# Performance work log

Hardware: AMD Instinct MI355X
Metric: run time of the kernel (lower is better)

Reference implementation:

```python
import jax, jax.numpy as jnp
import numpy as np

B, S, D = 2, 2048, 1024
H, DH = 16, 64          # n_heads, d_head = d_model // n_heads
WINDOW = 128            # sliding-window size (causal, includes self)


def setup_inputs() -> dict:
    key = jax.random.key(0)
    k1, k2, k3 = jax.random.split(key, 3)
    x = jax.random.normal(k1, (B, S, D), dtype=jnp.float32)
    w_qkv = jax.random.normal(k2, (D, 3 * D), dtype=jnp.float32) * (1.0 / np.sqrt(D))
    w_out = jax.random.normal(k3, (D, D), dtype=jnp.float32) * (1.0 / np.sqrt(D))
    return {"x": x, "w_qkv": w_qkv, "w_out": w_out}


def reference(x, w_qkv, w_out):
    b, s, d = x.shape
    # QKV projection (no bias): [B,S,3D] -> [B,S,3,H,DH]
    qkv = (x @ w_qkv).reshape(b, s, 3, H, DH)
    q, k, v = qkv[:, :, 0], qkv[:, :, 1], qkv[:, :, 2]  # each [B,S,H,DH]
    scale = 1.0 / np.sqrt(DH)
    # Dense scores [B,H,S,S], as the explicit-mask SDPA path computes
    scores = jnp.einsum("bihd,bjhd->bhij", q, k) * scale
    i = jnp.arange(s)[:, None]
    j = jnp.arange(s)[None, :]
    # allowed: causal AND within sliding window of WINDOW positions (incl. self)
    allowed = (j <= i) & (j > i - WINDOW)
    scores = jnp.where(allowed, scores, -jnp.inf)
    attn = jax.nn.softmax(scores, axis=-1)
    out = jnp.einsum("bhij,bjhd->bihd", attn, v).reshape(b, s, d)
    return out @ w_out
```

## Files before the change

kernel.cpp:

```cpp
#include <hip/hip_runtime.h>

#define SQ      2048
#define NB      2
#define NH      16
#define DHD     64
#define WIN     128
#define DMODEL  1024
#define TRIPLE  3072

typedef __attribute__((ext_vector_type(8))) short  short8;
typedef __attribute__((ext_vector_type(4))) float  f32x4;

__device__ __forceinline__ unsigned short f2bf(float f) {
  unsigned u = __float_as_uint(f);
  u += 0x7fff + ((u >> 16) & 1);
  return (unsigned short)(u >> 16);
}

__device__ __forceinline__ void load_lds16(const void* g, void* l) {
  __builtin_amdgcn_global_load_lds(
      (const __attribute__((address_space(1))) unsigned int*)g,
      (__attribute__((address_space(3))) unsigned int*)l, 16, 0, 0);
}

__global__ __launch_bounds__(256) void prep_kernel(
    const float* __restrict__ x, const float* __restrict__ w_qkv,
    const float* __restrict__ w_out,
    unsigned short* __restrict__ xb, unsigned short* __restrict__ wqkvT,
    unsigned short* __restrict__ woutT) {
  __shared__ float tile[32][33];
  int blk = blockIdx.x, tid = threadIdx.x;
  if (blk < 4096) {
    int idx = blk * 256 + tid;
    f32x4 v = ((const f32x4*)x)[idx];
    ushort4 o;
    o.x = f2bf(v[0]); o.y = f2bf(v[1]); o.z = f2bf(v[2]); o.w = f2bf(v[3]);
    ((ushort4*)xb)[idx] = o;
    return;
  }
  const float* in;
  unsigned short* out;
  int K = DMODEL, N, t;
  if (blk < 7168) { in = w_qkv; out = wqkvT; N = TRIPLE;  t = blk - 4096; }
  else            { in = w_out; out = woutT; N = DMODEL;  t = blk - 7168; }
  int ntiles = N / 32;
  int n0 = (t % ntiles) * 32, k0 = (t / ntiles) * 32;
  int tx = tid & 31, ty = tid >> 5;
#pragma unroll
  for (int r = 0; r < 4; ++r)
    tile[ty + 8 * r][tx] = in[(size_t)(k0 + ty + 8 * r) * N + (n0 + tx)];
  __syncthreads();
#pragma unroll
  for (int r = 0; r < 4; ++r)
    out[(size_t)(n0 + ty + 8 * r) * K + (k0 + tx)] = f2bf(tile[tx][ty + 8 * r]);
}

template <bool BF16OUT>
__global__ __launch_bounds__(512) void gemm_bt_kernel(
    const unsigned short* __restrict__ A,
    const unsigned short* __restrict__ Bt,
    void* __restrict__ Cv,
    int M, int N, int K) {
  __shared__ short lsA[128 * 64];
  __shared__ short lsB[128 * 64];
  int tid  = threadIdx.x;
  int wave = tid >> 6, lane = tid & 63;
  int quad = lane >> 4, l16 = lane & 15;
  int wm = (wave & 3) * 32;
  int wn = (wave >> 2) * 64;
  int m0 = blockIdx.x * 128, n0 = blockIdx.y * 128;

  f32x4 acc[2][4] = {};

  const short* Ag = (const short*)A;
  const short* Bg = (const short*)Bt;

  int row8 = lane >> 3;
  int gcol = ((lane & 7) ^ row8) * 8;
  int sw = (l16 & 7) * 8;

  for (int k0 = 0; k0 < K; k0 += 64) {
    const short* Ab = Ag + (size_t)(m0 + wave * 16) * K + k0;
    const short* Bb = Bg + (size_t)(n0 + wave * 16) * K + k0;
#pragma unroll
    for (int inst = 0; inst < 2; ++inst) {
      int r = inst * 8 + row8;
      load_lds16(Ab + (size_t)r * K + gcol, &lsA[(wave * 16 + inst * 8) * 64]);
      load_lds16(Bb + (size_t)r * K + gcol, &lsB[(wave * 16 + inst * 8) * 64]);
    }
    __syncthreads();
#pragma unroll
    for (int ks = 0; ks < 2; ++ks) {
      int coff = ((ks * 32 + quad * 8) ^ sw);
      short8 af[2], bf[4];
#pragma unroll
      for (int t = 0; t < 2; ++t)
        af[t] = *(const short8*)(&lsA[(wm + t * 16 + l16) * 64 + coff]);
#pragma unroll
      for (int t = 0; t < 4; ++t)
        bf[t] = *(const short8*)(&lsB[(wn + t * 16 + l16) * 64 + coff]);
#pragma unroll
      for (int mt = 0; mt < 2; ++mt)
#pragma unroll
        for (int nt = 0; nt < 4; ++nt)
          acc[mt][nt] = __builtin_amdgcn_mfma_f32_16x16x32_bf16(
              af[mt], bf[nt], acc[mt][nt], 0, 0, 0);
    }
    __syncthreads();
  }
#pragma unroll
  for (int mt = 0; mt < 2; ++mt)
#pragma unroll
    for (int nt = 0; nt < 4; ++nt)
#pragma unroll
      for (int r = 0; r < 4; ++r) {
        int row = m0 + wm + mt * 16 + quad * 4 + r;
        int col = n0 + wn + nt * 16 + l16;
        if (BF16OUT)
          ((unsigned short*)Cv)[(size_t)row * N + col] = f2bf(acc[mt][nt][r]);
        else
          ((float*)Cv)[(size_t)row * N + col] = acc[mt][nt][r];
      }
}

template <bool BF16OUT>
__global__ __launch_bounds__(512) void gemm_bt_n64_kernel(
    const unsigned short* __restrict__ A,
    const unsigned short* __restrict__ Bt,
    void* __restrict__ Cv,
    int M, int N, int K) {
  __shared__ short lsA[128 * 64];
  __shared__ short lsB[64 * 64];
  int tid  = threadIdx.x;
  int wave = tid >> 6, lane = tid & 63;
  int quad = lane >> 4, l16 = lane & 15;
  int wm = wave * 16;
  int m0 = blockIdx.x * 128, n0 = blockIdx.y * 64;

  f32x4 acc[4] = {};

  const short* Ag = (const short*)A;
  const short* Bg = (const short*)Bt;

  int row8 = lane >> 3;
  int gcol = ((lane & 7) ^ row8) * 8;
  int sw = (l16 & 7) * 8;

  for (int k0 = 0; k0 < K; k0 += 64) {
    const short* Ab = Ag + (size_t)(m0 + wave * 16) * K + k0;
    const short* Bb = Bg + (size_t)(n0 + wave * 8) * K + k0;
#pragma unroll
    for (int inst = 0; inst < 2; ++inst) {
      int r = inst * 8 + row8;
      load_lds16(Ab + (size_t)r * K + gcol, &lsA[(wave * 16 + inst * 8) * 64]);
    }
    load_lds16(Bb + (size_t)row8 * K + gcol, &lsB[(wave * 8) * 64]);
    __syncthreads();
#pragma unroll
    for (int ks = 0; ks < 2; ++ks) {
      int coff = ((ks * 32 + quad * 8) ^ sw);
      short8 af = *(const short8*)(&lsA[(wm + l16) * 64 + coff]);
#pragma unroll
      for (int nt = 0; nt < 4; ++nt) {
        short8 bf = *(const short8*)(&lsB[(nt * 16 + l16) * 64 + coff]);
        acc[nt] = __builtin_amdgcn_mfma_f32_16x16x32_bf16(af, bf, acc[nt], 0, 0, 0);
      }
    }
    __syncthreads();
  }
#pragma unroll
  for (int nt = 0; nt < 4; ++nt)
#pragma unroll
    for (int r = 0; r < 4; ++r) {
      int row = m0 + wm + quad * 4 + r;
      int col = n0 + nt * 16 + l16;
      if (BF16OUT)
        ((unsigned short*)Cv)[(size_t)row * N + col] = f2bf(acc[nt][r]);
      else
        ((float*)Cv)[(size_t)row * N + col] = acc[nt][r];
    }
}

#define KSTR 72
#define VSTR 200
#define PSTR 72
__global__ __launch_bounds__(256) void attn_kernel(
    const unsigned short* __restrict__ qkvb,
    unsigned short* __restrict__ attnout) {
  __shared__ short Kl[192 * KSTR];
  __shared__ short Vt[64 * VSTR];
  __shared__ short Pl[4][16 * PSTR];

  int i0 = blockIdx.x * 64, h = blockIdx.y, b = blockIdx.z;
  int tid = threadIdx.x, wave = tid >> 6, lane = tid & 63;
  int quad = lane >> 4, l16 = lane & 15;
  const unsigned short* base = qkvb + (size_t)b * SQ * TRIPLE;

  short8 qa[2];
  {
    int qi = i0 + wave * 16 + l16;
    const unsigned short* qrow = base + (size_t)qi * TRIPLE + h * DHD;
    qa[0] = *(const short8*)(qrow + quad * 8);
    qa[1] = *(const short8*)(qrow + 32 + quad * 8);
  }

  int jbase = (i0 >= WIN) ? (i0 - WIN) : 0;
  int nch = (i0 + 64 - jbase) >> 6;

  int srow_ = tid >> 3;
  int scol_ = (tid & 7) * 8;
  for (int p = 0; p < 2 * nch; ++p) {
    int r = p * 32 + srow_;
    int j = jbase + r;
    const unsigned short* kr = base + (size_t)j * TRIPLE + DMODEL + h * DHD + scol_;
    *(short8*)(&Kl[r * KSTR + scol_]) = *(const short8*)kr;
    const unsigned short* vr = base + (size_t)j * TRIPLE + 2 * DMODEL + h * DHD + scol_;
    short8 vv = *(const short8*)vr;
#pragma unroll
    for (int e = 0; e < 8; ++e) {
      int d = scol_ + e;
      Vt[d * VSTR + (r ^ (((d >> 3) & 7) << 3))] = vv[e];
    }
  }
  __syncthreads();

  f32x4 o[4] = {};
  float mrow[4] = {-1e30f, -1e30f, -1e30f, -1e30f};
  float lrow[4] = {0.f, 0.f, 0.f, 0.f};
  int irow = i0 + wave * 16 + quad * 4;

  for (int c = 0; c < nch; ++c) {
    int jc = jbase + c * 64;

    f32x4 s[4] = {};
#pragma unroll
    for (int ks = 0; ks < 2; ++ks)
#pragma unroll
      for (int nt = 0; nt < 4; ++nt) {
        short8 bk = *(const short8*)(&Kl[(c * 64 + nt * 16 + l16) * KSTR + ks * 32 + quad * 8]);
        s[nt] = __builtin_amdgcn_mfma_f32_16x16x32_bf16(qa[ks], bk, s[nt], 0, 0, 0);
      }
#pragma unroll
    for (int nt = 0; nt < 4; ++nt)
#pragma unroll
      for (int r = 0; r < 4; ++r) {
        int i_ = irow + r;
        int j_ = jc + nt * 16 + l16;
        bool ok = (j_ <= i_) && (j_ > i_ - WIN);
        s[nt][r] = ok ? s[nt][r] * 0.125f : -1e30f;
      }
    float rm[4];
#pragma unroll
    for (int r = 0; r < 4; ++r)
      rm[r] = fmaxf(fmaxf(s[0][r], s[1][r]), fmaxf(s[2][r], s[3][r]));
#pragma unroll
    for (int off = 1; off < 16; off <<= 1)
#pragma unroll
      for (int r = 0; r < 4; ++r) rm[r] = fmaxf(rm[r], __shfl_xor(rm[r], off, 64));
    float al[4];
#pragma unroll
    for (int r = 0; r < 4; ++r) {
      float mn = fmaxf(mrow[r], rm[r]);
      al[r] = __expf(mrow[r] - mn);
      mrow[r] = mn;
    }
    f32x4 p[4];
#pragma unroll
    for (int nt = 0; nt < 4; ++nt)
#pragma unroll
      for (int r = 0; r < 4; ++r) p[nt][r] = __expf(s[nt][r] - mrow[r]);
    float rs[4];
#pragma unroll
    for (int r = 0; r < 4; ++r)
      rs[r] = (p[0][r] + p[1][r]) + (p[2][r] + p[3][r]);
#pragma unroll
    for (int off = 1; off < 16; off <<= 1)
#pragma unroll
      for (int r = 0; r < 4; ++r) rs[r] += __shfl_xor(rs[r], off, 64);
#pragma unroll
    for (int r = 0; r < 4; ++r) lrow[r] = lrow[r] * al[r] + rs[r];
#pragma unroll
    for (int nt = 0; nt < 4; ++nt)
#pragma unroll
      for (int r = 0; r < 4; ++r) o[nt][r] *= al[r];
#pragma unroll
    for (int nt = 0; nt < 4; ++nt)
#pragma unroll
      for (int r = 0; r < 4; ++r)
        Pl[wave][(quad * 4 + r) * PSTR + nt * 16 + l16] = f2bf(p[nt][r]);
    short8 pa[2];
    pa[0] = *(const short8*)(&Pl[wave][l16 * PSTR + quad * 8]);
    pa[1] = *(const short8*)(&Pl[wave][l16 * PSTR + 32 + quad * 8]);
#pragma unroll
    for (int ks = 0; ks < 2; ++ks)
#pragma unroll
      for (int nt = 0; nt < 4; ++nt) {
        int d2 = nt * 16 + l16;
        int vsw = ((d2 >> 3) & 7) << 3;
        short8 bv = *(const short8*)(
            &Vt[d2 * VSTR + ((c * 64 + ks * 32 + quad * 8) ^ vsw)]);
        o[nt] = __builtin_amdgcn_mfma_f32_16x16x32_bf16(pa[ks], bv, o[nt], 0, 0, 0);
      }
  }

  float inv[4];
#pragma unroll
  for (int r = 0; r < 4; ++r) inv[r] = 1.0f / lrow[r];
#pragma unroll
  for (int nt = 0; nt < 4; ++nt)
#pragma unroll
    for (int r = 0; r < 4; ++r) {
      int i_ = irow + r;
      int d_ = nt * 16 + l16;
      attnout[(size_t)(b * SQ + i_) * DMODEL + h * DHD + d_] = f2bf(o[nt][r] * inv[r]);
    }
}

extern "C" void kernel_launch(void* const* d_in, const int* in_sizes, int n_in,
                              void* d_out, int out_size, void* d_ws, size_t ws_size,
                              hipStream_t stream) {
  const float* x     = (const float*)d_in[0];
  const float* w_qkv = (const float*)d_in[1];
  const float* w_out = (const float*)d_in[2];
  float* out = (float*)d_out;

  char* ws = (char*)d_ws;
  unsigned short* xb    = (unsigned short*)(ws);
  unsigned short* wqkvT = (unsigned short*)(ws + 8388608);
  unsigned short* woutT = (unsigned short*)(ws + 14680064);
  unsigned short* qkvb  = (unsigned short*)(ws + 16777216);
  unsigned short* attn  = (unsigned short*)(ws + 41943040);

  prep_kernel<<<8192, 256, 0, stream>>>(x, w_qkv, w_out, xb, wqkvT, woutT);
  gemm_bt_kernel<true><<<dim3((NB * SQ) / 128, TRIPLE / 128), 512, 0, stream>>>(
      xb, wqkvT, qkvb, NB * SQ, TRIPLE, DMODEL);
  attn_kernel<<<dim3(SQ / 64, NH, NB), 256, 0, stream>>>(qkvb, attn);
  gemm_bt_n64_kernel<false><<<dim3((NB * SQ) / 128, DMODEL / 64), 512, 0, stream>>>(
      attn, woutT, out, NB * SQ, DMODEL, DMODEL);
}
```

Baseline: 147.7 us.

## Replace QKV GEMM with 256x256 tiled, double-buffered, phase-scheduled kernel

Adds a new GEMM kernel for the QKV projection. It uses 256x256 output tiles, double-buffered LDS filled through global_load_lds, and XOR-swizzled LDS addressing. Each K tile is split into four barrier-separated phases so that LDS reads, asynchronous prefetch of the next tiles and MFMA run interleaved, with setprio around the MFMA blocks and a workgroup-id swizzle meant to improve L2 locality. The goal is higher arithmetic intensity and latency hiding compared with the 128x128 kernel. The trade-offs are heavy register pressure (128 accumulators per lane), 128 KB of LDS per block, and only 192 blocks for the device.

Result: slower. 151.5 us (+2.6%).

```diff
diff --git a/kernel.cpp b/kernel.cpp
--- a/kernel.cpp
+++ b/kernel.cpp
@@ -181,6 +181,138 @@
     }
 }
 
+template <int M, int N, int K, bool BF16OUT>
+__global__ __launch_bounds__(512) void gemm8p_kernel(
+    const unsigned short* __restrict__ A,
+    const unsigned short* __restrict__ Bt,
+    void* __restrict__ Cv) {
+  constexpr int NT  = K / 64;
+  constexpr int NBN = N / 256;
+  __shared__ short lsA[2][256 * 64];
+  __shared__ short lsB[2][256 * 64];
+
+  const int tid  = threadIdx.x;
+  const int wave = tid >> 6, lane = tid & 63;
+  const int quad = lane >> 4, l16 = lane & 15;
+  const int wm = (wave >> 2) * 128;
+  const int wn = (wave & 3) * 64;
+
+  const int nwg = gridDim.x;
+  const int swz = ((int)blockIdx.x & 7) * (nwg >> 3) + ((int)blockIdx.x >> 3);
+  const int m0 = (swz / NBN) * 256, n0 = (swz % NBN) * 256;
+
+  const short* Ag = (const short*)A + (size_t)m0 * K;
+  const short* Bg = (const short*)Bt + (size_t)n0 * K;
+
+  const int r8 = lane >> 3;
+  const int gc = ((lane & 7) ^ r8) * 8;
+  const int sw = (l16 & 7) * 8;
+  const int wrow = wave * 16;
+
+  f32x4 acc[8][4] = {};
+  short8 bf[4];
+
+#define SBAR0() __builtin_amdgcn_sched_barrier(0)
+#define PHASE_BAR()                                   \
+  do { SBAR0(); __builtin_amdgcn_s_barrier(); SBAR0(); } while (0)
+#define LGKM0()                                       \
+  do { asm volatile("s_waitcnt lgkmcnt(0)" ::: "memory"); SBAR0(); } while (0)
+#define WAITV(n) asm volatile("s_waitcnt vmcnt(" #n ")" ::: "memory")
+#define STAGE_HALF(lds, g)                                                        \
+  do {                                                                            \
+    load_lds16((g) + (size_t)(wrow + r8) * K + gc, (lds) + wrow * 64);            \
+    load_lds16((g) + (size_t)(wrow + 8 + r8) * K + gc, (lds) + (wrow + 8) * 64);  \
+  } while (0)
+#define ST_A(t, h) STAGE_HALF(&lsA[(t) & 1][(h) * (128 * 64)],                    \
+                              Ag + (size_t)((h) * 128) * K + (t) * 64)
+#define ST_B(t, h) STAGE_HALF(&lsB[(t) & 1][(h) * (128 * 64)],                    \
+                              Bg + (size_t)((h) * 128) * K + (t) * 64)
+
+#define PH_READS_A(mh, ks)                                                        \
+  { const int coff = ((ks) * 32 + quad * 8) ^ sw;                                 \
+    _Pragma("unroll") for (int i_ = 0; i_ < 4; ++i_)                              \
+      af[i_] = *(const short8*)(&la[(wm + (mh) * 64 + i_ * 16 + l16) * 64 + coff]); }
+#define PH_READS_B(ks)                                                            \
+  { const int coff = ((ks) * 32 + quad * 8) ^ sw;                                 \
+    _Pragma("unroll") for (int n_ = 0; n_ < 4; ++n_)                              \
+      bf[n_] = *(const short8*)(&lb[(wn + n_ * 16 + l16) * 64 + coff]); }
+#define PH_MFMA(base)                                                             \
+  __builtin_amdgcn_s_setprio(1);                                                  \
+  _Pragma("unroll") for (int i_ = 0; i_ < 4; ++i_)                                \
+    _Pragma("unroll") for (int n_ = 0; n_ < 4; ++n_)                              \
+      acc[(base) + i_][n_] = __builtin_amdgcn_mfma_f32_16x16x32_bf16(             \
+          af[i_], bf[n_], acc[(base) + i_][n_], 0, 0, 0);                         \
+  __builtin_amdgcn_s_setprio(0);
+
+#define TILE(t, DO_A1, DO_NX, W0, W3)                                             \
+  {                                                                               \
+    short* la = lsA[(t) & 1];                                                     \
+    short* lb = lsB[(t) & 1];                                                     \
+    short8 af[4];                                                                 \
+                                                     \
+    PH_READS_A(0, 0); PH_READS_B(0);                                              \
+    if (DO_A1) { ST_A((t) + 1, 1); }                                              \
+    PHASE_BAR(); LGKM0();                                                         \
+    PH_MFMA(0);                                                                   \
+    W0;                                                                           \
+    PHASE_BAR();                                                                  \
+                                                     \
+    PH_READS_A(1, 0);                                                             \
+    PHASE_BAR(); LGKM0();                                                         \
+    PH_MFMA(4);                                                                   \
+    PHASE_BAR();                                                                  \
+                                                     \
+    PH_READS_A(0, 1); PH_READS_B(1);                                              \
+    PHASE_BAR(); LGKM0();                                                         \
+    PH_MFMA(0);                                                                   \
+    PHASE_BAR();                                                                  \
+                                                     \
+    PH_READS_A(1, 1);                                                             \
+    if (DO_NX) { ST_A((t) + 2, 0); ST_B((t) + 2, 0); ST_B((t) + 2, 1); }          \
+    PHASE_BAR(); LGKM0();                                                         \
+    PH_MFMA(4);                                                                   \
+    W3;                                                                           \
+    PHASE_BAR();                                                                  \
+  }
+
+  ST_A(0, 0); ST_A(0, 1); ST_B(0, 0); ST_B(0, 1);
+  ST_A(1, 0); ST_B(1, 0); ST_B(1, 1);
+  WAITV(6);
+  PHASE_BAR();
+
+  TILE(0, true, true, ((void)0), WAITV(8));
+  for (int t = 1; t <= NT - 3; ++t)
+    TILE(t, true, true, WAITV(8), WAITV(8));
+  TILE(NT - 2, true, false, WAITV(8), WAITV(2));
+  TILE(NT - 1, false, false, WAITV(0), ((void)0));
+
+#undef TILE
+#undef PH_MFMA
+#undef PH_READS_B
+#undef PH_READS_A
+#undef ST_B
+#undef ST_A
+#undef STAGE_HALF
+#undef WAITV
+#undef LGKM0
+#undef PHASE_BAR
+#undef SBAR0
+
+#pragma unroll
+  for (int m = 0; m < 8; ++m)
+#pragma unroll
+    for (int n = 0; n < 4; ++n)
+#pragma unroll
+      for (int r = 0; r < 4; ++r) {
+        int row = m0 + wm + m * 16 + quad * 4 + r;
+        int col = n0 + wn + n * 16 + l16;
+        if (BF16OUT)
+          ((unsigned short*)Cv)[(size_t)row * N + col] = f2bf(acc[m][n][r]);
+        else
+          ((float*)Cv)[(size_t)row * N + col] = acc[m][n][r];
+      }
+}
+
 #define KSTR 72
 #define VSTR 200
 #define PSTR 72
@@ -332,8 +464,8 @@
   unsigned short* attn  = (unsigned short*)(ws + 41943040);
 
   prep_kernel<<<8192, 256, 0, stream>>>(x, w_qkv, w_out, xb, wqkvT, woutT);
-  gemm_bt_kernel<true><<<dim3((NB * SQ) / 128, TRIPLE / 128), 512, 0, stream>>>(
-      xb, wqkvT, qkvb, NB * SQ, TRIPLE, DMODEL);
+  gemm8p_kernel<NB * SQ, TRIPLE, DMODEL, true>
+      <<<(NB * SQ / 256) * (TRIPLE / 256), 512, 0, stream>>>(xb, wqkvT, qkvb);
   attn_kernel<<<dim3(SQ / 64, NH, NB), 256, 0, stream>>>(qkvb, attn);
   gemm_bt_n64_kernel<false><<<dim3((NB * SQ) / 128, DMODEL / 64), 512, 0, stream>>>(
       attn, woutT, out, NB * SQ, DMODEL, DMODEL);
```

## Process 128 query rows per attention block to reuse staged K/V tiles

Applied to the files above, without the earlier changes.

Each attention block now covers 128 query rows, split into two 64-row groups per wave, instead of 64. The staged K/V window grows from 192 to 256 keys, so the overlapping K/V rows are loaded once for both groups rather than twice, and per-wave chunk skipping avoids MFMA work on fully masked chunks. The trade-off is half as many blocks (512 instead of 1024), more LDS per block and more registers per wave, which may lower occupancy and parallelism.

Result: faster. 143.5 us (median of 2 runs) (-2.9%).

```diff
diff --git a/kernel.cpp b/kernel.cpp
--- a/kernel.cpp
+++ b/kernel.cpp
@@ -182,30 +182,31 @@
 }
 
 #define KSTR 72
-#define VSTR 200
+#define VSTR 264
 #define PSTR 72
 __global__ __launch_bounds__(256) void attn_kernel(
     const unsigned short* __restrict__ qkvb,
     unsigned short* __restrict__ attnout) {
-  __shared__ short Kl[192 * KSTR];
+  __shared__ short Kl[256 * KSTR];
   __shared__ short Vt[64 * VSTR];
   __shared__ short Pl[4][16 * PSTR];
 
-  int i0 = blockIdx.x * 64, h = blockIdx.y, b = blockIdx.z;
+  int i0 = blockIdx.x * 128, h = blockIdx.y, b = blockIdx.z;
   int tid = threadIdx.x, wave = tid >> 6, lane = tid & 63;
   int quad = lane >> 4, l16 = lane & 15;
   const unsigned short* base = qkvb + (size_t)b * SQ * TRIPLE;
 
-  short8 qa[2];
-  {
-    int qi = i0 + wave * 16 + l16;
+  short8 qa[2][2];
+#pragma unroll
+  for (int g = 0; g < 2; ++g) {
+    int qi = i0 + g * 64 + wave * 16 + l16;
     const unsigned short* qrow = base + (size_t)qi * TRIPLE + h * DHD;
-    qa[0] = *(const short8*)(qrow + quad * 8);
-    qa[1] = *(const short8*)(qrow + 32 + quad * 8);
+    qa[g][0] = *(const short8*)(qrow + quad * 8);
+    qa[g][1] = *(const short8*)(qrow + 32 + quad * 8);
   }
 
   int jbase = (i0 >= WIN) ? (i0 - WIN) : 0;
-  int nch = (i0 + 64 - jbase) >> 6;
+  int nch = (i0 + 128 - jbase) >> 6;
 
   int srow_ = tid >> 3;
   int scol_ = (tid & 7) * 8;
@@ -224,96 +225,110 @@
   }
   __syncthreads();
 
-  f32x4 o[4] = {};
-  float mrow[4] = {-1e30f, -1e30f, -1e30f, -1e30f};
-  float lrow[4] = {0.f, 0.f, 0.f, 0.f};
-  int irow = i0 + wave * 16 + quad * 4;
+  f32x4 o[2][4] = {};
+  float mrow[2][4], lrow[2][4];
+#pragma unroll
+  for (int g = 0; g < 2; ++g)
+#pragma unroll
+    for (int r = 0; r < 4; ++r) { mrow[g][r] = -1e30f; lrow[g][r] = 0.f; }
 
   for (int c = 0; c < nch; ++c) {
     int jc = jbase + c * 64;
-
-    f32x4 s[4] = {};
-#pragma unroll
-    for (int ks = 0; ks < 2; ++ks)
-#pragma unroll
-      for (int nt = 0; nt < 4; ++nt) {
-        short8 bk = *(const short8*)(&Kl[(c * 64 + nt * 16 + l16) * KSTR + ks * 32 + quad * 8]);
-        s[nt] = __builtin_amdgcn_mfma_f32_16x16x32_bf16(qa[ks], bk, s[nt], 0, 0, 0);
+#pragma unroll
+    for (int g = 0; g < 2; ++g) {
+      int ig = i0 + g * 64 + wave * 16;
+      if (jc > ig + 15) continue;
+      if (jc + 63 <= ig - WIN) continue;
+      int irow = ig + quad * 4;
+
+      f32x4 s[4] = {};
+#pragma unroll
+      for (int ks = 0; ks < 2; ++ks)
+#pragma unroll
+        for (int nt = 0; nt < 4; ++nt) {
+          short8 bk = *(const short8*)(
+              &Kl[(c * 64 + nt * 16 + l16) * KSTR + ks * 32 + quad * 8]);
+          s[nt] = __builtin_amdgcn_mfma_f32_16x16x32_bf16(qa[g][ks], bk, s[nt], 0, 0, 0);
+        }
+#pragma unroll
+      for (int nt = 0; nt < 4; ++nt)
+#pragma unroll
+        for (int r = 0; r < 4; ++r) {
+          int i_ = irow + r;
+          int j_ = jc + nt * 16 + l16;
+          bool ok = (j_ <= i_) && (j_ > i_ - WIN);
+          s[nt][r] = ok ? s[nt][r] * 0.125f : -1e30f;
+        }
+      float rm[4];
+#pragma unroll
+      for (int r = 0; r < 4; ++r)
+        rm[r] = fmaxf(fmaxf(s[0][r], s[1][r]), fmaxf(s[2][r], s[3][r]));
+#pragma unroll
+      for (int off = 1; off < 16; off <<= 1)
+#pragma unroll
+        for (int r = 0; r < 4; ++r) rm[r] = fmaxf(rm[r], __shfl_xor(rm[r], off, 64));
+      float al[4];
+#pragma unroll
+      for (int r = 0; r < 4; ++r) {
+        float mn = fmaxf(mrow[g][r], rm[r]);
+        al[r] = __expf(mrow[g][r] - mn);
+        mrow[g][r] = mn;
       }
+      f32x4 p[4];
+#pragma unroll
+      for (int nt = 0; nt < 4; ++nt)
+#pragma unroll
+        for (int r = 0; r < 4; ++r) p[nt][r] = __expf(s[nt][r] - mrow[g][r]);
+      float rs[4];
+#pragma unroll
+      for (int r = 0; r < 4; ++r)
+        rs[r] = (p[0][r] + p[1][r]) + (p[2][r] + p[3][r]);
+#pragma unroll
+      for (int off = 1; off < 16; off <<= 1)
+#pragma unroll
+        for (int r = 0; r < 4; ++r) rs[r] += __shfl_xor(rs[r], off, 64);
+#pragma unroll
+      for (int r = 0; r < 4; ++r) lrow[g][r] = lrow[g][r] * al[r] + rs[r];
+#pragma unroll
+      for (int nt = 0; nt < 4; ++nt)
+#pragma unroll
+        for (int r = 0; r < 4; ++r) o[g][nt][r] *= al[r];
+#pragma unroll
+      for (int nt = 0; nt < 4; ++nt)
+#pragma unroll
+        for (int r = 0; r < 4; ++r)
+          Pl[wave][(quad * 4 + r) * PSTR + nt * 16 + l16] = f2bf(p[nt][r]);
+      short8 pa[2];
+      pa[0] = *(const short8*)(&Pl[wave][l16 * PSTR + quad * 8]);
+      pa[1] = *(const short8*)(&Pl[wave][l16 * PSTR + 32 + quad * 8]);
+#pragma unroll
+      for (int ks = 0; ks < 2; ++ks)
+#pragma unroll
+        for (int nt = 0; nt < 4; ++nt) {
+          int d2 = nt * 16 + l16;
+          int vsw = ((d2 >> 3) & 7) << 3;
+          short8 bv = *(const short8*)(
+              &Vt[d2 * VSTR + ((c * 64 + ks * 32 + quad * 8) ^ vsw)]);
+          o[g][nt] = __builtin_amdgcn_mfma_f32_16x16x32_bf16(pa[ks], bv, o[g][nt], 0, 0, 0);
+        }
+    }
+  }
+
+#pragma unroll
+  for (int g = 0; g < 2; ++g) {
+    float inv[4];
+#pragma unroll
+    for (int r = 0; r < 4; ++r) inv[r] = 1.0f / lrow[g][r];
+    int ig = i0 + g * 64 + wave * 16 + quad * 4;
 #pragma unroll
     for (int nt = 0; nt < 4; ++nt)
 #pragma unroll
       for (int r = 0; r < 4; ++r) {
-        int i_ = irow + r;
-        int j_ = jc + nt * 16 + l16;
-        bool ok = (j_ <= i_) && (j_ > i_ - WIN);
-        s[nt][r] = ok ? s[nt][r] * 0.125f : -1e30f;
+        int i_ = ig + r;
+        int d_ = nt * 16 + l16;
+        attnout[(size_t)(b * SQ + i_) * DMODEL + h * DHD + d_] = f2bf(o[g][nt][r] * inv[r]);
       }
-    float rm[4];
-#pragma unroll
-    for (int r = 0; r < 4; ++r)
-      rm[r] = fmaxf(fmaxf(s[0][r], s[1][r]), fmaxf(s[2][r], s[3][r]));
-#pragma unroll
-    for (int off = 1; off < 16; off <<= 1)
-#pragma unroll
-      for (int r = 0; r < 4; ++r) rm[r] = fmaxf(rm[r], __shfl_xor(rm[r], off, 64));
-    float al[4];
-#pragma unroll
-    for (int r = 0; r < 4; ++r) {
-      float mn = fmaxf(mrow[r], rm[r]);
-      al[r] = __expf(mrow[r] - mn);
-      mrow[r] = mn;
-    }
-    f32x4 p[4];
-#pragma unroll
-    for (int nt = 0; nt < 4; ++nt)
-#pragma unroll
-      for (int r = 0; r < 4; ++r) p[nt][r] = __expf(s[nt][r] - mrow[r]);
-    float rs[4];
-#pragma unroll
-    for (int r = 0; r < 4; ++r)
-      rs[r] = (p[0][r] + p[1][r]) + (p[2][r] + p[3][r]);
-#pragma unroll
-    for (int off = 1; off < 16; off <<= 1)
-#pragma unroll
-      for (int r = 0; r < 4; ++r) rs[r] += __shfl_xor(rs[r], off, 64);
-#pragma unroll
-    for (int r = 0; r < 4; ++r) lrow[r] = lrow[r] * al[r] + rs[r];
-#pragma unroll
-    for (int nt = 0; nt < 4; ++nt)
-#pragma unroll
-      for (int r = 0; r < 4; ++r) o[nt][r] *= al[r];
-#pragma unroll
-    for (int nt = 0; nt < 4; ++nt)
-#pragma unroll
-      for (int r = 0; r < 4; ++r)
-        Pl[wave][(quad * 4 + r) * PSTR + nt * 16 + l16] = f2bf(p[nt][r]);
-    short8 pa[2];
-    pa[0] = *(const short8*)(&Pl[wave][l16 * PSTR + quad * 8]);
-    pa[1] = *(const short8*)(&Pl[wave][l16 * PSTR + 32 + quad * 8]);
-#pragma unroll
-    for (int ks = 0; ks < 2; ++ks)
-#pragma unroll
-      for (int nt = 0; nt < 4; ++nt) {
-        int d2 = nt * 16 + l16;
-        int vsw = ((d2 >> 3) & 7) << 3;
-        short8 bv = *(const short8*)(
-            &Vt[d2 * VSTR + ((c * 64 + ks * 32 + quad * 8) ^ vsw)]);
-        o[nt] = __builtin_amdgcn_mfma_f32_16x16x32_bf16(pa[ks], bv, o[nt], 0, 0, 0);
-      }
-  }
-
-  float inv[4];
-#pragma unroll
-  for (int r = 0; r < 4; ++r) inv[r] = 1.0f / lrow[r];
-#pragma unroll
-  for (int nt = 0; nt < 4; ++nt)
-#pragma unroll
-    for (int r = 0; r < 4; ++r) {
-      int i_ = irow + r;
-      int d_ = nt * 16 + l16;
-      attnout[(size_t)(b * SQ + i_) * DMODEL + h * DHD + d_] = f2bf(o[nt][r] * inv[r]);
-    }
+  }
 }
 
 extern "C" void kernel_launch(void* const* d_in, const int* in_sizes, int n_in,
@@ -334,7 +349,7 @@
   prep_kernel<<<8192, 256, 0, stream>>>(x, w_qkv, w_out, xb, wqkvT, woutT);
   gemm_bt_kernel<true><<<dim3((NB * SQ) / 128, TRIPLE / 128), 512, 0, stream>>>(
       xb, wqkvT, qkvb, NB * SQ, TRIPLE, DMODEL);
-  attn_kernel<<<dim3(SQ / 64, NH, NB), 256, 0, stream>>>(qkvb, attn);
+  attn_kernel<<<dim3(SQ / 128, NH, NB), 256, 0, stream>>>(qkvb, attn);
   gemm_bt_n64_kernel<false><<<dim3((NB * SQ) / 128, DMODEL / 64), 512, 0, stream>>>(
       attn, woutT, out, NB * SQ, DMODEL, DMODEL);
 }
```
